# Kernel optimization log

Hardware: AMD Instinct MI355X
Metric: run time of the kernel (lower is better)

Reference implementation:

```python
import jax, jax.numpy as jnp
import numpy as np

LN_EPS = 1e-5


def setup_inputs() -> dict:
    key = jax.random.key(0)
    k1, k2, k3, k4 = jax.random.split(key, 4)
    N, D, E = 10000, 512, 150000
    scale = 1.0 / np.sqrt(D)
    return {
        "node_feature": jax.random.normal(k1, (N, D), dtype=jnp.float32),
        "edge_index": jax.random.randint(k2, (2, E), 0, N, dtype=jnp.int64),
        "ln_gamma": jnp.ones((D,), dtype=jnp.float32),
        "ln_beta": jnp.zeros((D,), dtype=jnp.float32),
        "w_l": jax.random.normal(k3, (D, D), dtype=jnp.float32) * scale,
        "b_l": jnp.zeros((D,), dtype=jnp.float32),
        "w_r": jax.random.normal(k4, (D, D), dtype=jnp.float32) * scale,
    }


def reference(node_feature, edge_index, ln_gamma, ln_beta, w_l, b_l, w_r):
    N = node_feature.shape[0]
    residual = node_feature

    # LayerNorm over feature dim
    mu = jnp.mean(node_feature, axis=-1, keepdims=True)
    var = jnp.mean(jnp.square(node_feature - mu), axis=-1, keepdims=True)
    x = (node_feature - mu) * jax.lax.rsqrt(var + LN_EPS) * ln_gamma + ln_beta

    # SAGEConv (mean aggr): gather x_j from src, segment-mean into dst
    src, dst = edge_index[0], edge_index[1]
    msg = x[src]                                   # [E, D]
    summed = jax.ops.segment_sum(msg, dst, num_segments=N)        # [N, D]
    cnt = jax.ops.segment_sum(jnp.ones_like(dst, dtype=x.dtype), dst, num_segments=N)
    agg = summed / jnp.maximum(cnt, 1.0)[:, None]

    # out = lin_l(agg) + lin_r(x)  (lin_r has no bias in PyG SAGEConv)
    out = agg @ w_l.T + b_l + x @ w_r.T
    out = jax.nn.relu(out)
    # dropout is identity in eval mode
    return out + residual
```

## Files before the change

kernel.cpp:

```cpp
#include <hip/hip_runtime.h>
#include <hip/hip_bf16.h>

typedef float f32x4 __attribute__((ext_vector_type(4)));
typedef __bf16 bf16x8 __attribute__((ext_vector_type(8)));
typedef unsigned short u16x8 __attribute__((ext_vector_type(8)));

#define N_NODES 10000
#define DIM 512
#define MPAD 10112
#define DEGCAP 96

__global__ __launch_bounds__(256) void zero_kernel(int* __restrict__ cnt) {
    cnt[blockIdx.x * 256 + threadIdx.x] = 0;
}

__global__ __launch_bounds__(256) void phase1_kernel(
    const float* __restrict__ wl, const float* __restrict__ wr,
    __hip_bfloat16* __restrict__ W,
    const float* __restrict__ xin, const float* __restrict__ gamma,
    const float* __restrict__ beta, __hip_bfloat16* __restrict__ A,
    const int* __restrict__ eidx, int* __restrict__ cnt, int* __restrict__ adj,
    int E, int fill_start) {
    int b = blockIdx.x;
    int tid = threadIdx.x;

    if (b < 512) {
        int idx = b * 256 + tid;
        int base = idx * 4;
        int d = base >> 10;
        int k = base & 1023;
        const float* src = (k < 512) ? (wl + d * 512 + k) : (wr + d * 512 + (k - 512));
        float4 v = *(const float4*)src;
        __hip_bfloat16* o = W + (size_t)d * 1024 + k;
        o[0] = __float2bfloat16(v.x);
        o[1] = __float2bfloat16(v.y);
        o[2] = __float2bfloat16(v.z);
        o[3] = __float2bfloat16(v.w);
    } else if (b < fill_start) {
        int row = (b - 512) * 4 + (tid >> 6);
        int lane = tid & 63;
        const float* xr = xin + (size_t)row * DIM + lane * 8;
        float4 v0 = *(const float4*)xr;
        float4 v1 = *(const float4*)(xr + 4);
        float s  = v0.x + v0.y + v0.z + v0.w + v1.x + v1.y + v1.z + v1.w;
        float ss = v0.x*v0.x + v0.y*v0.y + v0.z*v0.z + v0.w*v0.w
                 + v1.x*v1.x + v1.y*v1.y + v1.z*v1.z + v1.w*v1.w;
        #pragma unroll
        for (int o = 32; o > 0; o >>= 1) {
            s  += __shfl_xor(s, o, 64);
            ss += __shfl_xor(ss, o, 64);
        }
        float mu  = s * (1.0f / 512.0f);
        float var = ss * (1.0f / 512.0f) - mu * mu;
        float rstd = rsqrtf(var + 1e-5f);
        float4 g0 = *(const float4*)(gamma + lane * 8);
        float4 g1 = *(const float4*)(gamma + lane * 8 + 4);
        float4 b0 = *(const float4*)(beta + lane * 8);
        float4 b1 = *(const float4*)(beta + lane * 8 + 4);
        __hip_bfloat16* a = A + (size_t)row * 1024 + 512 + lane * 8;
        a[0] = __float2bfloat16((v0.x - mu) * rstd * g0.x + b0.x);
        a[1] = __float2bfloat16((v0.y - mu) * rstd * g0.y + b0.y);
        a[2] = __float2bfloat16((v0.z - mu) * rstd * g0.z + b0.z);
        a[3] = __float2bfloat16((v0.w - mu) * rstd * g0.w + b0.w);
        a[4] = __float2bfloat16((v1.x - mu) * rstd * g1.x + b1.x);
        a[5] = __float2bfloat16((v1.y - mu) * rstd * g1.y + b1.y);
        a[6] = __float2bfloat16((v1.z - mu) * rstd * g1.z + b1.z);
        a[7] = __float2bfloat16((v1.w - mu) * rstd * g1.w + b1.w);
    } else {
        int i = (b - fill_start) * 256 + tid;
        if (i < E) {
            int dst = eidx[E + i];
            int src = eidx[i];
            int pos = atomicAdd(&cnt[dst], 1);
            if (pos < DEGCAP) adj[dst * DEGCAP + pos] = src;
        }
    }
}

__global__ __launch_bounds__(256) void gather_kernel(const int* __restrict__ cnt,
                                                     const int* __restrict__ adj,
                                                     __hip_bfloat16* __restrict__ A) {
    int gw = (blockIdx.x * 256 + threadIdx.x) >> 6;
    int lane = threadIdx.x & 63;
    int deg = cnt[gw];
    const int* al = adj + gw * DEGCAP;
    float acc0[8] = {}, acc1[8] = {};
    int j = 0;
    for (; j + 8 <= deg; j += 8) {
        int a0 = al[j], a1 = al[j+1], a2 = al[j+2], a3 = al[j+3];
        int a4 = al[j+4], a5 = al[j+5], a6 = al[j+6], a7 = al[j+7];
        u16x8 v0 = *(const u16x8*)(A + (size_t)a0 * 1024 + 512 + lane * 8);
        u16x8 v1 = *(const u16x8*)(A + (size_t)a1 * 1024 + 512 + lane * 8);
        u16x8 v2 = *(const u16x8*)(A + (size_t)a2 * 1024 + 512 + lane * 8);
        u16x8 v3 = *(const u16x8*)(A + (size_t)a3 * 1024 + 512 + lane * 8);
        u16x8 v4 = *(const u16x8*)(A + (size_t)a4 * 1024 + 512 + lane * 8);
        u16x8 v5 = *(const u16x8*)(A + (size_t)a5 * 1024 + 512 + lane * 8);
        u16x8 v6 = *(const u16x8*)(A + (size_t)a6 * 1024 + 512 + lane * 8);
        u16x8 v7 = *(const u16x8*)(A + (size_t)a7 * 1024 + 512 + lane * 8);
        #pragma unroll
        for (int k = 0; k < 8; ++k) {
            acc0[k] += __uint_as_float((unsigned)v0[k] << 16)
                     + __uint_as_float((unsigned)v1[k] << 16)
                     + __uint_as_float((unsigned)v2[k] << 16)
                     + __uint_as_float((unsigned)v3[k] << 16);
            acc1[k] += __uint_as_float((unsigned)v4[k] << 16)
                     + __uint_as_float((unsigned)v5[k] << 16)
                     + __uint_as_float((unsigned)v6[k] << 16)
                     + __uint_as_float((unsigned)v7[k] << 16);
        }
    }
    for (; j + 4 <= deg; j += 4) {
        int a0 = al[j], a1 = al[j+1], a2 = al[j+2], a3 = al[j+3];
        u16x8 v0 = *(const u16x8*)(A + (size_t)a0 * 1024 + 512 + lane * 8);
        u16x8 v1 = *(const u16x8*)(A + (size_t)a1 * 1024 + 512 + lane * 8);
        u16x8 v2 = *(const u16x8*)(A + (size_t)a2 * 1024 + 512 + lane * 8);
        u16x8 v3 = *(const u16x8*)(A + (size_t)a3 * 1024 + 512 + lane * 8);
        #pragma unroll
        for (int k = 0; k < 8; ++k) {
            acc0[k] += __uint_as_float((unsigned)v0[k] << 16)
                     + __uint_as_float((unsigned)v1[k] << 16);
            acc1[k] += __uint_as_float((unsigned)v2[k] << 16)
                     + __uint_as_float((unsigned)v3[k] << 16);
        }
    }
    for (; j < deg; ++j) {
        int a0 = al[j];
        u16x8 v0 = *(const u16x8*)(A + (size_t)a0 * 1024 + 512 + lane * 8);
        #pragma unroll
        for (int k = 0; k < 8; ++k)
            acc0[k] += __uint_as_float((unsigned)v0[k] << 16);
    }
    float sc = 1.0f / fmaxf((float)deg, 1.0f);
    __hip_bfloat16* o = A + (size_t)gw * 1024 + lane * 8;
    #pragma unroll
    for (int k = 0; k < 8; ++k)
        o[k] = __float2bfloat16((acc0[k] + acc1[k]) * sc);
}

__global__ __launch_bounds__(256) void gemm_kernel(const __hip_bfloat16* __restrict__ A,
                                                   const __hip_bfloat16* __restrict__ Wb,
                                                   const float* __restrict__ bias,
                                                   const float* __restrict__ resid,
                                                   float* __restrict__ out) {
    __shared__ __hip_bfloat16 As[2][64 * 32];
    __shared__ __hip_bfloat16 Bs[2][64 * 32];
    const int tid = threadIdx.x;
    const int lane = tid & 63;
    const int w = tid >> 6;
    const int wr = w >> 1, wc = w & 1;

    int bid = blockIdx.x;
    int tl = (bid & 7) * 158 + (bid >> 3);
    int mx = tl >> 3, ny = tl & 7;
    const size_t arow0 = (size_t)mx * 64;
    const size_t bcol0 = (size_t)ny * 64;

    f32x4 acc[2][2] = {};

    const int rsw = ((lane & 15) >> 1) & 3;
    const int csw = (((lane >> 4) ^ rsw) & 3) * 8;

#define STAGE(buf, t)                                                                \
    {                                                                                \
        int r = tid >> 2, sl = tid & 3;                                              \
        int c8 = sl ^ ((r >> 1) & 3);                                                \
        const __hip_bfloat16* ga = A + (size_t)(arow0 + r) * 1024 + (t) * 32 + c8 * 8; \
        __builtin_amdgcn_global_load_lds(                                            \
            (const __attribute__((address_space(1))) void*)ga,                       \
            (__attribute__((address_space(3))) void*)(As[buf] + tid * 8), 16, 0, 0); \
        const __hip_bfloat16* gb = Wb + (size_t)(bcol0 + r) * 1024 + (t) * 32 + c8 * 8; \
        __builtin_amdgcn_global_load_lds(                                            \
            (const __attribute__((address_space(1))) void*)gb,                       \
            (__attribute__((address_space(3))) void*)(Bs[buf] + tid * 8), 16, 0, 0); \
    }

    STAGE(0, 0)
    __syncthreads();

    for (int t = 0; t < 32; ++t) {
        int p = t & 1;
        if (t + 1 < 32) STAGE(p ^ 1, t + 1)

        bf16x8 af[2], bfr[2];
        #pragma unroll
        for (int m = 0; m < 2; ++m)
            af[m] = *(const bf16x8*)(As[p] + (wr * 32 + m * 16 + (lane & 15)) * 32 + csw);
        #pragma unroll
        for (int n = 0; n < 2; ++n)
            bfr[n] = *(const bf16x8*)(Bs[p] + (wc * 32 + n * 16 + (lane & 15)) * 32 + csw);
        #pragma unroll
        for (int m = 0; m < 2; ++m)
            #pragma unroll
            for (int n = 0; n < 2; ++n)
                acc[m][n] = __builtin_amdgcn_mfma_f32_16x16x32_bf16(af[m], bfr[n], acc[m][n], 0, 0, 0);
        __syncthreads();
    }
#undef STAGE

    #pragma unroll
    for (int m = 0; m < 2; ++m) {
        int rowb = (int)arow0 + wr * 32 + m * 16 + (lane >> 4) * 4;
        #pragma unroll
        for (int n = 0; n < 2; ++n) {
            int col = (int)bcol0 + wc * 32 + n * 16 + (lane & 15);
            float bv = bias[col];
            #pragma unroll
            for (int j = 0; j < 4; ++j) {
                int row = rowb + j;
                if (row < N_NODES) {
                    float v = acc[m][n][j] + bv;
                    v = v > 0.0f ? v : 0.0f;
                    out[(size_t)row * 512 + col] = v + resid[(size_t)row * 512 + col];
                }
            }
        }
    }
}

extern "C" void kernel_launch(void* const* d_in, const int* in_sizes, int n_in,
                              void* d_out, int out_size, void* d_ws, size_t ws_size,
                              hipStream_t stream) {
    const float* node  = (const float*)d_in[0];
    const int*   eidx  = (const int*)d_in[1];
    const float* gamma = (const float*)d_in[2];
    const float* beta  = (const float*)d_in[3];
    const float* wl    = (const float*)d_in[4];
    const float* bl    = (const float*)d_in[5];
    const float* wr    = (const float*)d_in[6];
    float* out = (float*)d_out;
    const int E = in_sizes[1] / 2;

    char* ws = (char*)d_ws;
    int* cnt = (int*)ws;
    int* adj = cnt + 10240;
    size_t adj_bytes = ((size_t)N_NODES * DEGCAP * 4 + 255) & ~(size_t)255;
    __hip_bfloat16* A = (__hip_bfloat16*)((char*)adj + adj_bytes);
    __hip_bfloat16* W = (__hip_bfloat16*)((char*)A + (size_t)MPAD * 1024 * 2);

    const int fill_start = 512 + 2500;
    const int nFill = (E + 255) / 256;

    zero_kernel<<<40, 256, 0, stream>>>(cnt);
    phase1_kernel<<<fill_start + nFill, 256, 0, stream>>>(
        wl, wr, W, node, gamma, beta, A, eidx, cnt, adj, E, fill_start);
    gather_kernel<<<(N_NODES * 64) / 256, 256, 0, stream>>>(cnt, adj, A);
    gemm_kernel<<<1264, 256, 0, stream>>>(A, W, bl, node, out);
}
```

Baseline: 71.85 us.

## Split GEMM K dimension across waves with per-wave LDS buffers and reduction

Rewrites the GEMM block so each of the 4 waves computes the full 64x64 output tile over a quarter of K (256), using private double-buffered LDS regions and no per-iteration block barriers. Partial accumulators are reduced through LDS at the end, and the epilogue is vectorized with float4 bias/residual/output accesses. This removes 32 __syncthreads per tile and widens each wave's MFMA work. In exchange it uses 64KB of LDS per block, which lowers occupancy, and adds a reduction pass.

```diff
diff --git a/kernel.cpp b/kernel.cpp
--- a/kernel.cpp
+++ b/kernel.cpp
@@ -142,12 +142,10 @@
                                                    const float* __restrict__ bias,
                                                    const float* __restrict__ resid,
                                                    float* __restrict__ out) {
-    __shared__ __hip_bfloat16 As[2][64 * 32];
-    __shared__ __hip_bfloat16 Bs[2][64 * 32];
+    __shared__ __hip_bfloat16 lds[4][8192];
     const int tid = threadIdx.x;
     const int lane = tid & 63;
     const int w = tid >> 6;
-    const int wr = w >> 1, wc = w & 1;
 
     int bid = blockIdx.x;
     int tl = (bid & 7) * 158 + (bid >> 3);
@@ -155,64 +153,103 @@
     const size_t arow0 = (size_t)mx * 64;
     const size_t bcol0 = (size_t)ny * 64;
 
-    f32x4 acc[2][2] = {};
+    __hip_bfloat16* Aw0 = &lds[w][0];
+    __hip_bfloat16* Bw0 = &lds[w][2048];
+    __hip_bfloat16* Aw1 = &lds[w][4096];
+    __hip_bfloat16* Bw1 = &lds[w][6144];
+    const int kw0 = w * 256;
+
+    f32x4 acc[4][4] = {};
 
     const int rsw = ((lane & 15) >> 1) & 3;
     const int csw = (((lane >> 4) ^ rsw) & 3) * 8;
-
-#define STAGE(buf, t)                                                                \
-    {                                                                                \
-        int r = tid >> 2, sl = tid & 3;                                              \
-        int c8 = sl ^ ((r >> 1) & 3);                                                \
-        const __hip_bfloat16* ga = A + (size_t)(arow0 + r) * 1024 + (t) * 32 + c8 * 8; \
-        __builtin_amdgcn_global_load_lds(                                            \
-            (const __attribute__((address_space(1))) void*)ga,                       \
-            (__attribute__((address_space(3))) void*)(As[buf] + tid * 8), 16, 0, 0); \
-        const __hip_bfloat16* gb = Wb + (size_t)(bcol0 + r) * 1024 + (t) * 32 + c8 * 8; \
-        __builtin_amdgcn_global_load_lds(                                            \
-            (const __attribute__((address_space(1))) void*)gb,                       \
-            (__attribute__((address_space(3))) void*)(Bs[buf] + tid * 8), 16, 0, 0); \
-    }
-
-    STAGE(0, 0)
+    const int srr = lane >> 2;
+    const int scc = lane & 3;
+
+#define STAGE(bufA, bufB, kb)                                                          \
+    {                                                                                  \
+        _Pragma("unroll")                                                              \
+        for (int it = 0; it < 4; ++it) {                                               \
+            int rr = it * 16 + srr;                                                    \
+            int c8 = scc ^ ((rr >> 1) & 3);                                            \
+            const __hip_bfloat16* ga = A + (size_t)(arow0 + rr) * 1024 + (kb) + c8 * 8; \
+            __builtin_amdgcn_global_load_lds(                                          \
+                (const __attribute__((address_space(1))) void*)ga,                     \
+                (__attribute__((address_space(3))) void*)((bufA) + it * 512 + lane * 8), 16, 0, 0); \
+        }                                                                              \
+        _Pragma("unroll")                                                              \
+        for (int it = 0; it < 4; ++it) {                                               \
+            int rr = it * 16 + srr;                                                    \
+            int c8 = scc ^ ((rr >> 1) & 3);                                            \
+            const __hip_bfloat16* gb = Wb + (size_t)(bcol0 + rr) * 1024 + (kb) + c8 * 8; \
+            __builtin_amdgcn_global_load_lds(                                          \
+                (const __attribute__((address_space(1))) void*)gb,                     \
+                (__attribute__((address_space(3))) void*)((bufB) + it * 512 + lane * 8), 16, 0, 0); \
+        }                                                                              \
+    }
+
+    STAGE(Aw0, Bw0, kw0)
+
+    #pragma unroll 1
+    for (int t = 0; t < 8; ++t) {
+        const __hip_bfloat16* pa = (t & 1) ? Aw1 : Aw0;
+        const __hip_bfloat16* pb = (t & 1) ? Bw1 : Bw0;
+        if (t + 1 < 8) {
+            __hip_bfloat16* na = (t & 1) ? Aw0 : Aw1;
+            __hip_bfloat16* nb = (t & 1) ? Bw0 : Bw1;
+            STAGE(na, nb, kw0 + (t + 1) * 32)
+            asm volatile("s_waitcnt vmcnt(8)" ::: "memory");
+        } else {
+            asm volatile("s_waitcnt vmcnt(0)" ::: "memory");
+        }
+        bf16x8 af[4], bfr[4];
+        #pragma unroll
+        for (int m = 0; m < 4; ++m)
+            af[m] = *(const bf16x8*)(pa + (m * 16 + (lane & 15)) * 32 + csw);
+        #pragma unroll
+        for (int n = 0; n < 4; ++n)
+            bfr[n] = *(const bf16x8*)(pb + (n * 16 + (lane & 15)) * 32 + csw);
+        #pragma unroll
+        for (int m = 0; m < 4; ++m)
+            #pragma unroll
+            for (int n = 0; n < 4; ++n)
+                acc[m][n] = __builtin_amdgcn_mfma_f32_16x16x32_bf16(af[m], bfr[n], acc[m][n], 0, 0, 0);
+    }
+#undef STAGE
+
+    float* red = (float*)&lds[0][0];
+    float* myred = red + w * 4096;
+    const int coli = lane & 15;
+    const int rowi0 = (lane >> 4) * 4;
+    #pragma unroll
+    for (int m = 0; m < 4; ++m)
+        #pragma unroll
+        for (int n = 0; n < 4; ++n)
+            #pragma unroll
+            for (int j = 0; j < 4; ++j)
+                myred[(m * 16 + rowi0 + j) * 64 + n * 16 + coli] = acc[m][n][j];
     __syncthreads();
 
-    for (int t = 0; t < 32; ++t) {
-        int p = t & 1;
-        if (t + 1 < 32) STAGE(p ^ 1, t + 1)
-
-        bf16x8 af[2], bfr[2];
-        #pragma unroll
-        for (int m = 0; m < 2; ++m)
-            af[m] = *(const bf16x8*)(As[p] + (wr * 32 + m * 16 + (lane & 15)) * 32 + csw);
-        #pragma unroll
-        for (int n = 0; n < 2; ++n)
-            bfr[n] = *(const bf16x8*)(Bs[p] + (wc * 32 + n * 16 + (lane & 15)) * 32 + csw);
-        #pragma unroll
-        for (int m = 0; m < 2; ++m)
-            #pragma unroll
-            for (int n = 0; n < 2; ++n)
-                acc[m][n] = __builtin_amdgcn_mfma_f32_16x16x32_bf16(af[m], bfr[n], acc[m][n], 0, 0, 0);
-        __syncthreads();
-    }
-#undef STAGE
-
     #pragma unroll
-    for (int m = 0; m < 2; ++m) {
-        int rowb = (int)arow0 + wr * 32 + m * 16 + (lane >> 4) * 4;
-        #pragma unroll
-        for (int n = 0; n < 2; ++n) {
-            int col = (int)bcol0 + wc * 32 + n * 16 + (lane & 15);
-            float bv = bias[col];
-            #pragma unroll
-            for (int j = 0; j < 4; ++j) {
-                int row = rowb + j;
-                if (row < N_NODES) {
-                    float v = acc[m][n][j] + bv;
-                    v = v > 0.0f ? v : 0.0f;
-                    out[(size_t)row * 512 + col] = v + resid[(size_t)row * 512 + col];
-                }
-            }
+    for (int g = 0; g < 4; ++g) {
+        int e = g * 1024 + tid * 4;
+        int row = e >> 6;
+        int col = e & 63;
+        int grow = (int)arow0 + row;
+        if (grow < N_NODES) {
+            f32x4 s = *(const f32x4*)(red + e)
+                    + *(const f32x4*)(red + 4096 + e)
+                    + *(const f32x4*)(red + 8192 + e)
+                    + *(const f32x4*)(red + 12288 + e);
+            int gcol = (int)bcol0 + col;
+            float4 bv = *(const float4*)(bias + gcol);
+            float4 rv = *(const float4*)(resid + (size_t)grow * 512 + gcol);
+            float4 o;
+            o.x = fmaxf(s[0] + bv.x, 0.f) + rv.x;
+            o.y = fmaxf(s[1] + bv.y, 0.f) + rv.y;
+            o.z = fmaxf(s[2] + bv.z, 0.f) + rv.z;
+            o.w = fmaxf(s[3] + bv.w, 0.f) + rv.w;
+            *(float4*)(out + (size_t)grow * 512 + gcol) = o;
         }
     }
 }
```

Measured after the change: 72.19 us. Within noise of the previous version (+0.5%).
